# Optimization experiments

Hardware: AMD Instinct MI355X
Metric: run time of the kernel (lower is better)

Reference implementation:

```python
import jax, jax.numpy as jnp
import numpy as np

SEQ, B, I, H, L = 2048, 32, 1024, 1024, 2


def setup_inputs() -> dict:
    key = jax.random.key(0)
    ks = jax.random.split(key, 6)
    k = 1.0 / np.sqrt(H)
    x = jax.random.normal(ks[0], (SEQ, B, I), dtype=jnp.float32)
    h0 = jnp.zeros((L, B, H), dtype=jnp.float32)
    # layer 0 W_ih is [H, I]; with I == H all layers stack to [L, H, H]
    W_ih = jax.random.uniform(ks[1], (L, H, H), minval=-k, maxval=k, dtype=jnp.float32)
    W_hh = jax.random.uniform(ks[2], (L, H, H), minval=-k, maxval=k, dtype=jnp.float32)
    b_ih = jax.random.uniform(ks[3], (L, H), minval=-k, maxval=k, dtype=jnp.float32)
    b_hh = jax.random.uniform(ks[4], (L, H), minval=-k, maxval=k, dtype=jnp.float32)
    return {"x": x, "h0": h0, "W_ih": W_ih, "W_hh": W_hh, "b_ih": b_ih, "b_hh": b_hh}


def reference(x, h0, W_ih, W_hh, b_ih, b_hh):
    """Stacked tanh RNN, seq-first input [T, B, I]. Returns (h_history [T,B,H], h_T [L,B,H])."""
    num_layers = W_ih.shape[0]

    def step(h_prev, x_t):
        inp = x_t
        hs = []
        for l in range(num_layers):  # small fixed layer count
            a = (jnp.einsum('bd,cd->bc', inp, W_ih[l])
                 + jnp.einsum('bd,cd->bc', h_prev[l], W_hh[l])
                 + b_ih[l] + b_hh[l])
            hl = jnp.tanh(a)
            hs.append(hl)
            inp = hl
        h_new = jnp.stack(hs)  # [L, B, H]
        return h_new, h_new[-1]

    h_T, h_history = jax.lax.scan(step, h0, x)
    return h_history, h_T
```

## Files before the change

### kernel.cpp

```cpp
#include <hip/hip_runtime.h>
#include <stdint.h>

#define T_SEQ 2048
#define NB 32
#define NH 1024
#define HH (NH*NH)
#define HIST_ELEMS ((size_t)T_SEQ*NB*NH)
#define TEAM 32

typedef __attribute__((ext_vector_type(8))) short bf16x8;
typedef __attribute__((ext_vector_type(4))) float f32x4;
typedef __attribute__((ext_vector_type(4))) int   i32x4;
typedef __attribute__((ext_vector_type(2))) int   i32x2;
typedef __attribute__((ext_vector_type(4))) short s16x4;

__device__ __forceinline__ unsigned short bf16rne(float f){
  union { float f; unsigned u; } v; v.f = f;
  unsigned u = v.u;
  return (unsigned short)((u + 0x7FFFu + ((u >> 16) & 1u)) >> 16);
}
__device__ __forceinline__ float bf16tof(unsigned short s){
  union { unsigned u; float f; } v; v.u = ((unsigned)s) << 16; return v.f;
}
__device__ __forceinline__ float fast_tanh(float x){
  float ax = fabsf(x);
  float e  = __expf(-2.0f*ax);
  float t  = (1.0f - e) / (1.0f + e);
  return copysignf(t, x);
}

__device__ __forceinline__ i32x4 ld128_c(const void* p){
  i32x4 d;
  asm volatile("global_load_dwordx4 %0, %1, off sc0 sc1" : "=v"(d) : "v"(p) : "memory");
  return d;
}
__device__ __forceinline__ void st64_c(void* p, i32x2 v){
  asm volatile("global_store_dwordx2 %0, %1, off sc0 sc1" :: "v"(p), "v"(v) : "memory");
}
__device__ __forceinline__ void st32_c(void* p, unsigned v){
  asm volatile("global_store_dword %0, %1, off sc0 sc1" :: "v"(p), "v"(v) : "memory");
}
__device__ __forceinline__ unsigned ld32_c(const void* p){
  unsigned d;
  asm volatile("global_load_dword %0, %1, off sc0 sc1\n\ts_waitcnt vmcnt(0)"
               : "=v"(d) : "v"(p) : "memory");
  __builtin_amdgcn_sched_barrier(0);
  return d;
}
__device__ __forceinline__ void vmem_drain(){
  asm volatile("s_waitcnt vmcnt(0)" ::: "memory");
  __builtin_amdgcn_sched_barrier(0);
}

__global__ __launch_bounds__(256)
void pre_gemm(const float* __restrict__ x,
              const float* __restrict__ Wih,
              const float* __restrict__ bih,
              const float* __restrict__ bhh,
              _Float16* __restrict__ pre0)
{
  __shared__ float As[128][36];
  const int tid  = threadIdx.x;
  const int lane = tid & 63;
  const int wave = tid >> 6;
  const int l15  = lane & 15;
  const int l4   = lane >> 4;
  const int n0   = blockIdx.x * 128;
  const int m0   = blockIdx.y * 128;
  const int qm   = wave >> 1;
  const int qn   = wave & 1;

  f32x4 acc[4][4];
  #pragma unroll
  for (int i = 0; i < 4; ++i)
    #pragma unroll
    for (int j = 0; j < 4; ++j) acc[i][j] = (f32x4){0.f,0.f,0.f,0.f};

  const int sr = tid >> 1;
  const int sh = tid & 1;
  const float* xrow = x + (size_t)(m0 + sr)*NH + sh*16;

  for (int kb = 0; kb < 32; ++kb){
    __syncthreads();
    {
      const float* src = xrow + kb*32;
      f32x4 v0 = *(const f32x4*)(src + 0);
      f32x4 v1 = *(const f32x4*)(src + 4);
      f32x4 v2 = *(const f32x4*)(src + 8);
      f32x4 v3 = *(const f32x4*)(src + 12);
      float* dst = &As[sr][sh*16];
      *(f32x4*)(dst + 0)  = v0;
      *(f32x4*)(dst + 4)  = v1;
      *(f32x4*)(dst + 8)  = v2;
      *(f32x4*)(dst + 12) = v3;
    }
    __syncthreads();

    bf16x8 ahi[4], alo[4];
    #pragma unroll
    for (int mt = 0; mt < 4; ++mt){
      const float* ap = &As[64*qm + 16*mt + l15][l4*8];
      #pragma unroll
      for (int j = 0; j < 8; ++j){
        float a = ap[j];
        unsigned short hb = bf16rne(a);
        ahi[mt][j] = (short)hb;
        alo[mt][j] = (short)bf16rne(a - bf16tof(hb));
      }
    }
    #pragma unroll
    for (int nf = 0; nf < 4; ++nf){
      const int c = n0 + 64*qn + 16*nf + l15;
      const float* wp = Wih + (size_t)c*NH + kb*32 + l4*8;
      bf16x8 bf;
      #pragma unroll
      for (int j = 0; j < 8; ++j) bf[j] = (short)bf16rne(wp[j]);
      #pragma unroll
      for (int mt = 0; mt < 4; ++mt){
        acc[mt][nf] = __builtin_amdgcn_mfma_f32_16x16x32_bf16(ahi[mt], bf, acc[mt][nf], 0,0,0);
        acc[mt][nf] = __builtin_amdgcn_mfma_f32_16x16x32_bf16(alo[mt], bf, acc[mt][nf], 0,0,0);
      }
    }
  }

  #pragma unroll
  for (int nf = 0; nf < 4; ++nf){
    const int c = n0 + 64*qn + 16*nf + l15;
    const float bv = bih[c] + bhh[c];
    #pragma unroll
    for (int mt = 0; mt < 4; ++mt){
      const int mb = m0 + 64*qm + 16*mt + l4*4;
      #pragma unroll
      for (int j = 0; j < 4; ++j)
        pre0[(size_t)(mb + j)*NH + c] = (_Float16)(acc[mt][nf][j] + bv);
    }
  }
}

__global__ __launch_bounds__(256, 1)
void rnn_seq(const float* __restrict__ h0in,
             const float* __restrict__ Wih,
             const float* __restrict__ Whh,
             const float* __restrict__ bih,
             const float* __restrict__ bhh,
             const _Float16* __restrict__ pre0,
             float* __restrict__ dout,
             char* __restrict__ ws)
{
  const int tid  = threadIdx.x;
  const int lane = tid & 63;
  const int wave = tid >> 6;
  const int l15  = lane & 15;
  const int l4   = lane >> 4;

  unsigned* counts = (unsigned*)ws;
  unsigned* winner = (unsigned*)(ws + 64);
  unsigned* bcast  = (unsigned*)(ws + 128);
  unsigned* flags  = (unsigned*)(ws + 4096);
  char* h0buf = ws + 8192;
  char* h1buf = ws + 8192 + 131072;

  __shared__ unsigned sh_go, sh_rank, sh_base;

  if (tid == 0){
    unsigned xcc;
    asm volatile("s_getreg_b32 %0, hwreg(HW_REG_XCC_ID)" : "=s"(xcc));
    xcc &= 7u;
    unsigned slot = atomicAdd(&counts[xcc], 1u);
    unsigned go = 0, rank = 0, base = 0;
    if (slot < TEAM){
      if (slot == TEAM - 1) atomicCAS(winner, 0u, xcc + 1u);
      unsigned w = 0; long c = 0;
      for (;;){
        w = ld32_c(winner);
        if (w) break;
        if (++c > (1L << 20)) break;
        __builtin_amdgcn_s_sleep(8);
      }
      if (w == xcc + 1u){ go = 1; rank = slot; }
    }
    if (go){
      if (rank == 0){
        unsigned mx = 0;
        for (int i = 0; i < TEAM; ++i){ unsigned v = ld32_c(flags + i); if (v > mx) mx = v; }
        if (mx > 0xF0000000u) mx = 0;
        for (int i = 0; i < TEAM; ++i) st32_c(flags + i, mx);
        st32_c(bcast + 0, mx);
        vmem_drain();
        st32_c(bcast + 1, 1u);
        vmem_drain();
        base = mx;
      } else {
        long c = 0;
        for (;;){
          unsigned r = ld32_c(bcast + 1);
          if (r) break;
          if (++c > (1L << 23)) break;
          __builtin_amdgcn_s_sleep(2);
        }
        base = ld32_c(bcast + 0);
      }
    }
    sh_go = go; sh_rank = rank; sh_base = base;
  }
  __syncthreads();
  if (!sh_go) return;
  const unsigned rank = sh_rank;
  const unsigned base = sh_base;
  const int c0 = (int)rank * 32;

  bf16x8 wA[3][2][8];
  #pragma unroll
  for (int cf = 0; cf < 2; ++cf){
    const size_t row = (size_t)(c0 + cf*16 + l15) * NH;
    const float* s0 = Whh + row;
    const float* s1 = Wih + HH + row;
    const float* s2 = Whh + HH + row;
    #pragma unroll
    for (int s = 0; s < 8; ++s){
      const int k = wave*256 + s*32 + l4*8;
      #pragma unroll
      for (int j = 0; j < 8; ++j){
        wA[0][cf][s][j] = (short)bf16rne(s0[k+j]);
        wA[1][cf][s][j] = (short)bf16rne(s1[k+j]);
        wA[2][cf][s][j] = (short)bf16rne(s2[k+j]);
      }
    }
  }

  const int eb   = tid >> 3;
  const int ecb  = tid & 7;
  const int ecol = c0 + ecb*4;

  f32x4 bias1;
  #pragma unroll
  for (int j = 0; j < 4; ++j)
    bias1[j] = bih[NH + ecol + j] + bhh[NH + ecol + j];

  {
    const float* hs0 = h0in + (size_t)eb*NH + ecol;
    const float* hs1 = h0in + (size_t)NB*NH + (size_t)eb*NH + ecol;
    i32x2 p0, p1;
    p0[0] = (int)bf16rne(hs0[0]) | ((int)bf16rne(hs0[1]) << 16);
    p0[1] = (int)bf16rne(hs0[2]) | ((int)bf16rne(hs0[3]) << 16);
    p1[0] = (int)bf16rne(hs1[0]) | ((int)bf16rne(hs1[1]) << 16);
    p1[1] = (int)bf16rne(hs1[2]) | ((int)bf16rne(hs1[3]) << 16);
    st64_c(h0buf + 65536 + eb*2048 + ecol*2, p0);
    st64_c(h1buf + 65536 + eb*2048 + ecol*2, p1);
  }
  vmem_drain();
  __syncthreads();
  if (tid == 0) st32_c(flags + rank, base + 1u);

  __shared__ float scr[4][8][16][20];
  long spins = 0;

  for (int p = 0; p <= T_SEQ; ++p){
    const bool doL0 = (p < T_SEQ);
    const bool doL1 = (p >= 1);

    s16x4 praw = {0,0,0,0};
    if (doL0)
      praw = *(const s16x4*)(pre0 + (size_t)p*(NB*NH) + (size_t)eb*NH + ecol);

    if (wave == 0){
      const unsigned target = base + 1u + (unsigned)p;
      const unsigned* fp = flags + ((lane & 7) << 2);
      for (;;){
        i32x4 f = ld128_c(fp);
        vmem_drain();
        int ok = ((unsigned)f[0] >= target) && ((unsigned)f[1] >= target)
              && ((unsigned)f[2] >= target) && ((unsigned)f[3] >= target);
        if (__all(ok)) break;
        if (++spins > (1L << 25)) break;
        __builtin_amdgcn_s_sleep(1);
      }
    }
    __syncthreads();

    const char* h0rd = h0buf + ((p-1)&1)*65536;
    const char* h1rd = h1buf + ((p-2)&1)*65536;
    i32x4 g0[2][8], g1[2][8];
    #pragma unroll
    for (int bt = 0; bt < 2; ++bt){
      const int b = bt*16 + l15;
      #pragma unroll
      for (int s = 0; s < 8; ++s){
        const int d = wave*256 + s*32 + l4*8;
        g0[bt][s] = ld128_c(h0rd + b*2048 + d*2);
      }
    }
    if (doL1){
      #pragma unroll
      for (int bt = 0; bt < 2; ++bt){
        const int b = bt*16 + l15;
        #pragma unroll
        for (int s = 0; s < 8; ++s){
          const int d = wave*256 + s*32 + l4*8;
          g1[bt][s] = ld128_c(h1rd + b*2048 + d*2);
        }
      }
    }
    vmem_drain();

    f32x4 acc0[2][2] = {{{0,0,0,0},{0,0,0,0}},{{0,0,0,0},{0,0,0,0}}};
    f32x4 acc1[2][2] = {{{0,0,0,0},{0,0,0,0}},{{0,0,0,0},{0,0,0,0}}};
    #pragma unroll
    for (int cf = 0; cf < 2; ++cf){
      #pragma unroll
      for (int bt = 0; bt < 2; ++bt){
        #pragma unroll
        for (int s = 0; s < 8; ++s){
          bf16x8 b0 = __builtin_bit_cast(bf16x8, g0[bt][s]);
          if (doL0)
            acc0[cf][bt] = __builtin_amdgcn_mfma_f32_16x16x32_bf16(wA[0][cf][s], b0, acc0[cf][bt], 0,0,0);
          if (doL1){
            acc1[cf][bt] = __builtin_amdgcn_mfma_f32_16x16x32_bf16(wA[1][cf][s], b0, acc1[cf][bt], 0,0,0);
            bf16x8 b1 = __builtin_bit_cast(bf16x8, g1[bt][s]);
            acc1[cf][bt] = __builtin_amdgcn_mfma_f32_16x16x32_bf16(wA[2][cf][s], b1, acc1[cf][bt], 0,0,0);
          }
        }
      }
    }

    #pragma unroll
    for (int cf = 0; cf < 2; ++cf){
      #pragma unroll
      for (int bt = 0; bt < 2; ++bt){
        *(f32x4*)&scr[wave][(cf<<1)|bt][l15][l4*4]     = acc0[cf][bt];
        *(f32x4*)&scr[wave][4|(cf<<1)|bt][l15][l4*4]   = acc1[cf][bt];
      }
    }
    __syncthreads();

    const int fL0 = ((ecb >> 2) << 1) | (eb >> 4);
    f32x4 s0v = {0,0,0,0}, s1v = {0,0,0,0};
    #pragma unroll
    for (int w = 0; w < 4; ++w){
      s0v += *(const f32x4*)&scr[w][fL0][eb & 15][(ecb & 3)*4];
      s1v += *(const f32x4*)&scr[w][4|fL0][eb & 15][(ecb & 3)*4];
    }

    float hv0[4], hv1[4];
    if (doL0){
      union { s16x4 v; _Float16 h[4]; } pu; pu.v = praw;
      #pragma unroll
      for (int j = 0; j < 4; ++j)
        hv0[j] = fast_tanh(s0v[j] + (float)pu.h[j]);
      i32x2 pk;
      pk[0] = (int)bf16rne(hv0[0]) | ((int)bf16rne(hv0[1]) << 16);
      pk[1] = (int)bf16rne(hv0[2]) | ((int)bf16rne(hv0[3]) << 16);
      st64_c(h0buf + (p&1)*65536 + eb*2048 + ecol*2, pk);
    }
    if (doL1){
      #pragma unroll
      for (int j = 0; j < 4; ++j)
        hv1[j] = fast_tanh(s1v[j] + bias1[j]);
      i32x2 pk;
      pk[0] = (int)bf16rne(hv1[0]) | ((int)bf16rne(hv1[1]) << 16);
      pk[1] = (int)bf16rne(hv1[2]) | ((int)bf16rne(hv1[3]) << 16);
      st64_c(h1buf + ((p-1)&1)*65536 + eb*2048 + ecol*2, pk);
    }

    vmem_drain();
    __syncthreads();
    if (tid == 0) st32_c(flags + rank, base + 2u + (unsigned)p);

    if (doL1){
      f32x4 o = {hv1[0], hv1[1], hv1[2], hv1[3]};
      *(f32x4*)(dout + (size_t)(p-1)*(NB*NH) + (size_t)eb*NH + ecol) = o;
      if (p == T_SEQ)
        *(f32x4*)(dout + HIST_ELEMS + (size_t)NB*NH + (size_t)eb*NH + ecol) = o;
    }
    if (doL0 && p == T_SEQ-1){
      f32x4 o = {hv0[0], hv0[1], hv0[2], hv0[3]};
      *(f32x4*)(dout + HIST_ELEMS + (size_t)eb*NH + ecol) = o;
    }
  }
}

extern "C" void kernel_launch(void* const* d_in, const int* in_sizes, int n_in,
                              void* d_out, int out_size, void* d_ws, size_t ws_size,
                              hipStream_t stream)
{
  (void)in_sizes; (void)n_in; (void)out_size;
  const float* x   = (const float*)d_in[0];
  const float* h0  = (const float*)d_in[1];
  const float* Wih = (const float*)d_in[2];
  const float* Whh = (const float*)d_in[3];
  const float* bih = (const float*)d_in[4];
  const float* bhh = (const float*)d_in[5];
  float* out = (float*)d_out;
  char*  ws  = (char*)d_ws;

  const size_t PRE0_OFF = (size_t)1 << 20;
  const size_t NEED = PRE0_OFF + (size_t)T_SEQ*NB*NH*sizeof(_Float16);
  if (ws_size < NEED) return;

  _Float16* pre0 = (_Float16*)(ws + PRE0_OFF);

  hipMemsetAsync(ws, 0, 256, stream);
  pre_gemm<<<dim3(8, 512), 256, 0, stream>>>(x, Wih, bih, bhh, pre0);
  rnn_seq<<<dim3(512), 256, 0, stream>>>(h0, Wih, Whh, bih, bhh, pre0, out, ws);
}
```

Before: 15.42 ms.

## Replace flag barrier with tagged hidden-state words and launch only team blocks

The per-step flag barrier (stores, drain, flag write, then a wave spinning on every block's flag) is replaced by storing each bf16 hidden value next to a 16-bit step tag in 32-bit words. Readers poll the state buffer directly until all tags match the expected step. The XCC-team election is also dropped, so exactly 32 blocks are launched and rank comes from blockIdx. This removes a full round trip per step but doubles the state traffic, and it relies on all 32 blocks being co-resident and on the tags being written atomically with the data. A larger workspace region now has to be zeroed each call.

```diff
diff --git a/kernel.cpp b/kernel.cpp
--- a/kernel.cpp
+++ b/kernel.cpp
@@ -7,11 +7,11 @@
 #define HH (NH*NH)
 #define HIST_ELEMS ((size_t)T_SEQ*NB*NH)
 #define TEAM 32
+#define SLOT (NB*NH*4)
 
 typedef __attribute__((ext_vector_type(8))) short bf16x8;
 typedef __attribute__((ext_vector_type(4))) float f32x4;
 typedef __attribute__((ext_vector_type(4))) int   i32x4;
-typedef __attribute__((ext_vector_type(2))) int   i32x2;
 typedef __attribute__((ext_vector_type(4))) short s16x4;
 
 __device__ __forceinline__ unsigned short bf16rne(float f){
@@ -29,27 +29,17 @@
   return copysignf(t, x);
 }
 
-__device__ __forceinline__ i32x4 ld128_c(const void* p){
-  i32x4 d;
-  asm volatile("global_load_dwordx4 %0, %1, off sc0 sc1" : "=v"(d) : "v"(p) : "memory");
-  return d;
-}
-__device__ __forceinline__ void st64_c(void* p, i32x2 v){
-  asm volatile("global_store_dwordx2 %0, %1, off sc0 sc1" :: "v"(p), "v"(v) : "memory");
-}
-__device__ __forceinline__ void st32_c(void* p, unsigned v){
-  asm volatile("global_store_dword %0, %1, off sc0 sc1" :: "v"(p), "v"(v) : "memory");
-}
-__device__ __forceinline__ unsigned ld32_c(const void* p){
-  unsigned d;
-  asm volatile("global_load_dword %0, %1, off sc0 sc1\n\ts_waitcnt vmcnt(0)"
-               : "=v"(d) : "v"(p) : "memory");
-  __builtin_amdgcn_sched_barrier(0);
-  return d;
-}
-__device__ __forceinline__ void vmem_drain(){
-  asm volatile("s_waitcnt vmcnt(0)" ::: "memory");
-  __builtin_amdgcn_sched_barrier(0);
+__device__ __forceinline__ uint64_t ld_state(const uint64_t* p){
+  return __hip_atomic_load(p, __ATOMIC_RELAXED, __HIP_MEMORY_SCOPE_AGENT);
+}
+__device__ __forceinline__ void st_state(uint64_t* p, uint64_t v){
+  __hip_atomic_store(p, v, __ATOMIC_RELAXED, __HIP_MEMORY_SCOPE_AGENT);
+}
+
+__device__ __forceinline__ unsigned frag_word(uint64_t w, unsigned rep, unsigned &bad){
+  unsigned lo = (unsigned)w, hi = (unsigned)(w >> 32);
+  bad |= (((lo & 0xFFFFu) | (hi << 16)) ^ rep);
+  return (lo >> 16) | (hi & 0xFFFF0000u);
 }
 
 __global__ __launch_bounds__(256)
@@ -152,62 +142,11 @@
   const int wave = tid >> 6;
   const int l15  = lane & 15;
   const int l4   = lane >> 4;
-
-  unsigned* counts = (unsigned*)ws;
-  unsigned* winner = (unsigned*)(ws + 64);
-  unsigned* bcast  = (unsigned*)(ws + 128);
-  unsigned* flags  = (unsigned*)(ws + 4096);
-  char* h0buf = ws + 8192;
-  char* h1buf = ws + 8192 + 131072;
-
-  __shared__ unsigned sh_go, sh_rank, sh_base;
-
-  if (tid == 0){
-    unsigned xcc;
-    asm volatile("s_getreg_b32 %0, hwreg(HW_REG_XCC_ID)" : "=s"(xcc));
-    xcc &= 7u;
-    unsigned slot = atomicAdd(&counts[xcc], 1u);
-    unsigned go = 0, rank = 0, base = 0;
-    if (slot < TEAM){
-      if (slot == TEAM - 1) atomicCAS(winner, 0u, xcc + 1u);
-      unsigned w = 0; long c = 0;
-      for (;;){
-        w = ld32_c(winner);
-        if (w) break;
-        if (++c > (1L << 20)) break;
-        __builtin_amdgcn_s_sleep(8);
-      }
-      if (w == xcc + 1u){ go = 1; rank = slot; }
-    }
-    if (go){
-      if (rank == 0){
-        unsigned mx = 0;
-        for (int i = 0; i < TEAM; ++i){ unsigned v = ld32_c(flags + i); if (v > mx) mx = v; }
-        if (mx > 0xF0000000u) mx = 0;
-        for (int i = 0; i < TEAM; ++i) st32_c(flags + i, mx);
-        st32_c(bcast + 0, mx);
-        vmem_drain();
-        st32_c(bcast + 1, 1u);
-        vmem_drain();
-        base = mx;
-      } else {
-        long c = 0;
-        for (;;){
-          unsigned r = ld32_c(bcast + 1);
-          if (r) break;
-          if (++c > (1L << 23)) break;
-          __builtin_amdgcn_s_sleep(2);
-        }
-        base = ld32_c(bcast + 0);
-      }
-    }
-    sh_go = go; sh_rank = rank; sh_base = base;
-  }
-  __syncthreads();
-  if (!sh_go) return;
-  const unsigned rank = sh_rank;
-  const unsigned base = sh_base;
-  const int c0 = (int)rank * 32;
+  const int rank = blockIdx.x;
+  const int c0   = rank * 32;
+
+  char* H0 = ws + 4096;
+  char* H1 = ws + 4096 + 2*SLOT;
 
   bf16x8 wA[3][2][8];
   #pragma unroll
@@ -240,20 +179,21 @@
   {
     const float* hs0 = h0in + (size_t)eb*NH + ecol;
     const float* hs1 = h0in + (size_t)NB*NH + (size_t)eb*NH + ecol;
-    i32x2 p0, p1;
-    p0[0] = (int)bf16rne(hs0[0]) | ((int)bf16rne(hs0[1]) << 16);
-    p0[1] = (int)bf16rne(hs0[2]) | ((int)bf16rne(hs0[3]) << 16);
-    p1[0] = (int)bf16rne(hs1[0]) | ((int)bf16rne(hs1[1]) << 16);
-    p1[1] = (int)bf16rne(hs1[2]) | ((int)bf16rne(hs1[3]) << 16);
-    st64_c(h0buf + 65536 + eb*2048 + ecol*2, p0);
-    st64_c(h1buf + 65536 + eb*2048 + ecol*2, p1);
-  }
-  vmem_drain();
-  __syncthreads();
-  if (tid == 0) st32_c(flags + rank, base + 1u);
+    #pragma unroll
+    for (int half = 0; half < 2; ++half){
+      unsigned a0 = (((unsigned)bf16rne(hs0[2*half]))   << 16) | 1u;
+      unsigned a1 = (((unsigned)bf16rne(hs0[2*half+1])) << 16) | 1u;
+      unsigned b0 = (((unsigned)bf16rne(hs1[2*half]))   << 16) | 1u;
+      unsigned b1 = (((unsigned)bf16rne(hs1[2*half+1])) << 16) | 1u;
+      st_state((uint64_t*)(H0 + SLOT + (size_t)(eb*NH + ecol + 2*half)*4),
+               (uint64_t)a0 | ((uint64_t)a1 << 32));
+      st_state((uint64_t*)(H1 + SLOT + (size_t)(eb*NH + ecol + 2*half)*4),
+               (uint64_t)b0 | ((uint64_t)b1 << 32));
+    }
+  }
 
   __shared__ float scr[4][8][16][20];
-  long spins = 0;
+  long budget = 1L << 17;
 
   for (int p = 0; p <= T_SEQ; ++p){
     const bool doL0 = (p < T_SEQ);
@@ -263,45 +203,64 @@
     if (doL0)
       praw = *(const s16x4*)(pre0 + (size_t)p*(NB*NH) + (size_t)eb*NH + ecol);
 
-    if (wave == 0){
-      const unsigned target = base + 1u + (unsigned)p;
-      const unsigned* fp = flags + ((lane & 7) << 2);
-      for (;;){
-        i32x4 f = ld128_c(fp);
-        vmem_drain();
-        int ok = ((unsigned)f[0] >= target) && ((unsigned)f[1] >= target)
-              && ((unsigned)f[2] >= target) && ((unsigned)f[3] >= target);
-        if (__all(ok)) break;
-        if (++spins > (1L << 25)) break;
-        __builtin_amdgcn_s_sleep(1);
-      }
-    }
-    __syncthreads();
-
-    const char* h0rd = h0buf + ((p-1)&1)*65536;
-    const char* h1rd = h1buf + ((p-2)&1)*65536;
-    i32x4 g0[2][8], g1[2][8];
-    #pragma unroll
-    for (int bt = 0; bt < 2; ++bt){
-      const int b = bt*16 + l15;
-      #pragma unroll
-      for (int s = 0; s < 8; ++s){
-        const int d = wave*256 + s*32 + l4*8;
-        g0[bt][s] = ld128_c(h0rd + b*2048 + d*2);
-      }
-    }
-    if (doL1){
-      #pragma unroll
-      for (int bt = 0; bt < 2; ++bt){
-        const int b = bt*16 + l15;
+    const unsigned rep0 = (unsigned)(p + 1) * 0x10001u;
+    const unsigned rep1 = (unsigned)p       * 0x10001u;
+    const char* h0rd = H0 + (size_t)((p-1)&1)*SLOT;
+    const char* h1rd = H1 + (size_t)((p-2)&1)*SLOT;
+
+    i32x4 f0[2][8], f1[2][8];
+    bool need0 = true, need1 = doL1;
+    int round = 0;
+    while (need0 || need1){
+      if (need0){
+        unsigned bad = 0;
         #pragma unroll
-        for (int s = 0; s < 8; ++s){
-          const int d = wave*256 + s*32 + l4*8;
-          g1[bt][s] = ld128_c(h1rd + b*2048 + d*2);
+        for (int bt = 0; bt < 2; ++bt){
+          const uint64_t* rb =
+            (const uint64_t*)(h0rd + (size_t)(bt*16 + l15)*4096 + wave*1024 + l4*32);
+          #pragma unroll
+          for (int s = 0; s < 8; ++s){
+            uint64_t w0 = ld_state(rb + s*16 + 0);
+            uint64_t w1 = ld_state(rb + s*16 + 1);
+            uint64_t w2 = ld_state(rb + s*16 + 2);
+            uint64_t w3 = ld_state(rb + s*16 + 3);
+            i32x4 f;
+            f[0] = (int)frag_word(w0, rep0, bad);
+            f[1] = (int)frag_word(w1, rep0, bad);
+            f[2] = (int)frag_word(w2, rep0, bad);
+            f[3] = (int)frag_word(w3, rep0, bad);
+            f0[bt][s] = f;
+          }
         }
-      }
-    }
-    vmem_drain();
+        if (__all((int)(bad == 0))) need0 = false;
+      }
+      if (need1){
+        unsigned bad = 0;
+        #pragma unroll
+        for (int bt = 0; bt < 2; ++bt){
+          const uint64_t* rb =
+            (const uint64_t*)(h1rd + (size_t)(bt*16 + l15)*4096 + wave*1024 + l4*32);
+          #pragma unroll
+          for (int s = 0; s < 8; ++s){
+            uint64_t w0 = ld_state(rb + s*16 + 0);
+            uint64_t w1 = ld_state(rb + s*16 + 1);
+            uint64_t w2 = ld_state(rb + s*16 + 2);
+            uint64_t w3 = ld_state(rb + s*16 + 3);
+            i32x4 f;
+            f[0] = (int)frag_word(w0, rep1, bad);
+            f[1] = (int)frag_word(w1, rep1, bad);
+            f[2] = (int)frag_word(w2, rep1, bad);
+            f[3] = (int)frag_word(w3, rep1, bad);
+            f1[bt][s] = f;
+          }
+        }
+        if (__all((int)(bad == 0))) need1 = false;
+      }
+      if (need0 || need1){
+        if (--budget < 0) break;
+        if (++round > 2) __builtin_amdgcn_s_sleep(1);
+      }
+    }
 
     f32x4 acc0[2][2] = {{{0,0,0,0},{0,0,0,0}},{{0,0,0,0},{0,0,0,0}}};
     f32x4 acc1[2][2] = {{{0,0,0,0},{0,0,0,0}},{{0,0,0,0},{0,0,0,0}}};
@@ -311,24 +270,25 @@
       for (int bt = 0; bt < 2; ++bt){
         #pragma unroll
         for (int s = 0; s < 8; ++s){
-          bf16x8 b0 = __builtin_bit_cast(bf16x8, g0[bt][s]);
+          bf16x8 b0 = __builtin_bit_cast(bf16x8, f0[bt][s]);
           if (doL0)
             acc0[cf][bt] = __builtin_amdgcn_mfma_f32_16x16x32_bf16(wA[0][cf][s], b0, acc0[cf][bt], 0,0,0);
           if (doL1){
             acc1[cf][bt] = __builtin_amdgcn_mfma_f32_16x16x32_bf16(wA[1][cf][s], b0, acc1[cf][bt], 0,0,0);
-            bf16x8 b1 = __builtin_bit_cast(bf16x8, g1[bt][s]);
+            bf16x8 b1 = __builtin_bit_cast(bf16x8, f1[bt][s]);
             acc1[cf][bt] = __builtin_amdgcn_mfma_f32_16x16x32_bf16(wA[2][cf][s], b1, acc1[cf][bt], 0,0,0);
           }
         }
       }
     }
 
+    __syncthreads();
     #pragma unroll
     for (int cf = 0; cf < 2; ++cf){
       #pragma unroll
       for (int bt = 0; bt < 2; ++bt){
-        *(f32x4*)&scr[wave][(cf<<1)|bt][l15][l4*4]     = acc0[cf][bt];
-        *(f32x4*)&scr[wave][4|(cf<<1)|bt][l15][l4*4]   = acc1[cf][bt];
+        *(f32x4*)&scr[wave][(cf<<1)|bt][l15][l4*4]   = acc0[cf][bt];
+        *(f32x4*)&scr[wave][4|(cf<<1)|bt][l15][l4*4] = acc1[cf][bt];
       }
     }
     __syncthreads();
@@ -341,30 +301,34 @@
       s1v += *(const f32x4*)&scr[w][4|fL0][eb & 15][(ecb & 3)*4];
     }
 
+    const unsigned wtag0 = (unsigned)(p + 2);
+    const unsigned wtag1 = (unsigned)(p + 1);
     float hv0[4], hv1[4];
     if (doL0){
       union { s16x4 v; _Float16 h[4]; } pu; pu.v = praw;
       #pragma unroll
       for (int j = 0; j < 4; ++j)
         hv0[j] = fast_tanh(s0v[j] + (float)pu.h[j]);
-      i32x2 pk;
-      pk[0] = (int)bf16rne(hv0[0]) | ((int)bf16rne(hv0[1]) << 16);
-      pk[1] = (int)bf16rne(hv0[2]) | ((int)bf16rne(hv0[3]) << 16);
-      st64_c(h0buf + (p&1)*65536 + eb*2048 + ecol*2, pk);
+      char* wb = H0 + (size_t)(p&1)*SLOT + (size_t)(eb*NH + ecol)*4;
+      #pragma unroll
+      for (int half = 0; half < 2; ++half){
+        unsigned a0 = (((unsigned)bf16rne(hv0[2*half]))   << 16) | wtag0;
+        unsigned a1 = (((unsigned)bf16rne(hv0[2*half+1])) << 16) | wtag0;
+        st_state((uint64_t*)(wb + 8*half), (uint64_t)a0 | ((uint64_t)a1 << 32));
+      }
     }
     if (doL1){
       #pragma unroll
       for (int j = 0; j < 4; ++j)
         hv1[j] = fast_tanh(s1v[j] + bias1[j]);
-      i32x2 pk;
-      pk[0] = (int)bf16rne(hv1[0]) | ((int)bf16rne(hv1[1]) << 16);
-      pk[1] = (int)bf16rne(hv1[2]) | ((int)bf16rne(hv1[3]) << 16);
-      st64_c(h1buf + ((p-1)&1)*65536 + eb*2048 + ecol*2, pk);
-    }
-
-    vmem_drain();
-    __syncthreads();
-    if (tid == 0) st32_c(flags + rank, base + 2u + (unsigned)p);
+      char* wb = H1 + (size_t)((p-1)&1)*SLOT + (size_t)(eb*NH + ecol)*4;
+      #pragma unroll
+      for (int half = 0; half < 2; ++half){
+        unsigned a0 = (((unsigned)bf16rne(hv1[2*half]))   << 16) | wtag1;
+        unsigned a1 = (((unsigned)bf16rne(hv1[2*half+1])) << 16) | wtag1;
+        st_state((uint64_t*)(wb + 8*half), (uint64_t)a0 | ((uint64_t)a1 << 32));
+      }
+    }
 
     if (doL1){
       f32x4 o = {hv1[0], hv1[1], hv1[2], hv1[3]};
@@ -399,7 +363,7 @@
 
   _Float16* pre0 = (_Float16*)(ws + PRE0_OFF);
 
-  hipMemsetAsync(ws, 0, 256, stream);
+  hipMemsetAsync(ws, 0, 4096 + 4*(size_t)SLOT, stream);
   pre_gemm<<<dim3(8, 512), 256, 0, stream>>>(x, Wih, bih, bhh, pre0);
-  rnn_seq<<<dim3(512), 256, 0, stream>>>(h0, Wih, Whh, bih, bhh, pre0, out, ws);
-}
+  rnn_seq<<<dim3(TEAM), 256, 0, stream>>>(h0, Wih, Whh, bih, bhh, pre0, out, ws);
+}
```

Measured after the change: 46.18 ms. 3x slower.

## Replace XCC team election with direct 32-block launch and per-wave atomic flags

Applied to the files above, without the earlier changes.

The kernel now launches exactly 32 blocks instead of 512 and drops the XCC-local team election and base broadcast. Blocks therefore may land on different XCCs rather than sharing one. The per-step barrier now has each wave atomically bump its block's counter (each on its own 128-byte slot) and every wave poll all 32 counters itself. This removes two __syncthreads per step and the base-offset handshake. In exchange, cross-XCC traffic through coherent memory may be slower, and the spin now hot-polls before it sleeps.

```diff
diff --git a/kernel.cpp b/kernel.cpp
--- a/kernel.cpp
+++ b/kernel.cpp
@@ -36,9 +36,6 @@
 }
 __device__ __forceinline__ void st64_c(void* p, i32x2 v){
   asm volatile("global_store_dwordx2 %0, %1, off sc0 sc1" :: "v"(p), "v"(v) : "memory");
-}
-__device__ __forceinline__ void st32_c(void* p, unsigned v){
-  asm volatile("global_store_dword %0, %1, off sc0 sc1" :: "v"(p), "v"(v) : "memory");
 }
 __device__ __forceinline__ unsigned ld32_c(const void* p){
   unsigned d;
@@ -152,62 +149,12 @@
   const int wave = tid >> 6;
   const int l15  = lane & 15;
   const int l4   = lane >> 4;
-
-  unsigned* counts = (unsigned*)ws;
-  unsigned* winner = (unsigned*)(ws + 64);
-  unsigned* bcast  = (unsigned*)(ws + 128);
-  unsigned* flags  = (unsigned*)(ws + 4096);
-  char* h0buf = ws + 8192;
-  char* h1buf = ws + 8192 + 131072;
-
-  __shared__ unsigned sh_go, sh_rank, sh_base;
-
-  if (tid == 0){
-    unsigned xcc;
-    asm volatile("s_getreg_b32 %0, hwreg(HW_REG_XCC_ID)" : "=s"(xcc));
-    xcc &= 7u;
-    unsigned slot = atomicAdd(&counts[xcc], 1u);
-    unsigned go = 0, rank = 0, base = 0;
-    if (slot < TEAM){
-      if (slot == TEAM - 1) atomicCAS(winner, 0u, xcc + 1u);
-      unsigned w = 0; long c = 0;
-      for (;;){
-        w = ld32_c(winner);
-        if (w) break;
-        if (++c > (1L << 20)) break;
-        __builtin_amdgcn_s_sleep(8);
-      }
-      if (w == xcc + 1u){ go = 1; rank = slot; }
-    }
-    if (go){
-      if (rank == 0){
-        unsigned mx = 0;
-        for (int i = 0; i < TEAM; ++i){ unsigned v = ld32_c(flags + i); if (v > mx) mx = v; }
-        if (mx > 0xF0000000u) mx = 0;
-        for (int i = 0; i < TEAM; ++i) st32_c(flags + i, mx);
-        st32_c(bcast + 0, mx);
-        vmem_drain();
-        st32_c(bcast + 1, 1u);
-        vmem_drain();
-        base = mx;
-      } else {
-        long c = 0;
-        for (;;){
-          unsigned r = ld32_c(bcast + 1);
-          if (r) break;
-          if (++c > (1L << 23)) break;
-          __builtin_amdgcn_s_sleep(2);
-        }
-        base = ld32_c(bcast + 0);
-      }
-    }
-    sh_go = go; sh_rank = rank; sh_base = base;
-  }
-  __syncthreads();
-  if (!sh_go) return;
-  const unsigned rank = sh_rank;
-  const unsigned base = sh_base;
-  const int c0 = (int)rank * 32;
+  const int rank = blockIdx.x;
+  const int c0   = rank * 32;
+
+  unsigned* flags = (unsigned*)ws;
+  char* H0 = ws + 8192;
+  char* H1 = ws + 8192 + 131072;
 
   bf16x8 wA[3][2][8];
   #pragma unroll
@@ -245,12 +192,11 @@
     p0[1] = (int)bf16rne(hs0[2]) | ((int)bf16rne(hs0[3]) << 16);
     p1[0] = (int)bf16rne(hs1[0]) | ((int)bf16rne(hs1[1]) << 16);
     p1[1] = (int)bf16rne(hs1[2]) | ((int)bf16rne(hs1[3]) << 16);
-    st64_c(h0buf + 65536 + eb*2048 + ecol*2, p0);
-    st64_c(h1buf + 65536 + eb*2048 + ecol*2, p1);
+    st64_c(H0 + 65536 + eb*2048 + ecol*2, p0);
+    st64_c(H1 + 65536 + eb*2048 + ecol*2, p1);
   }
   vmem_drain();
-  __syncthreads();
-  if (tid == 0) st32_c(flags + rank, base + 1u);
+  if (lane == 0) atomicAdd(&flags[rank*32], 1u);
 
   __shared__ float scr[4][8][16][20];
   long spins = 0;
@@ -263,23 +209,20 @@
     if (doL0)
       praw = *(const s16x4*)(pre0 + (size_t)p*(NB*NH) + (size_t)eb*NH + ecol);
 
-    if (wave == 0){
-      const unsigned target = base + 1u + (unsigned)p;
-      const unsigned* fp = flags + ((lane & 7) << 2);
+    {
+      const unsigned target = 4u * (unsigned)(p + 1);
+      const unsigned* fp = flags + (lane & 31)*32;
       for (;;){
-        i32x4 f = ld128_c(fp);
-        vmem_drain();
-        int ok = ((unsigned)f[0] >= target) && ((unsigned)f[1] >= target)
-              && ((unsigned)f[2] >= target) && ((unsigned)f[3] >= target);
+        unsigned f = ld32_c(fp);
+        int ok = (lane >= 32) || (f >= target);
         if (__all(ok)) break;
-        if (++spins > (1L << 25)) break;
-        __builtin_amdgcn_s_sleep(1);
-      }
-    }
-    __syncthreads();
-
-    const char* h0rd = h0buf + ((p-1)&1)*65536;
-    const char* h1rd = h1buf + ((p-2)&1)*65536;
+        if (++spins > (1L << 21)) break;
+        if (spins > 4096) __builtin_amdgcn_s_sleep(1);
+      }
+    }
+
+    const char* h0rd = H0 + ((p-1)&1)*65536;
+    const char* h1rd = H1 + ((p-2)&1)*65536;
     i32x4 g0[2][8], g1[2][8];
     #pragma unroll
     for (int bt = 0; bt < 2; ++bt){
@@ -327,8 +270,8 @@
     for (int cf = 0; cf < 2; ++cf){
       #pragma unroll
       for (int bt = 0; bt < 2; ++bt){
-        *(f32x4*)&scr[wave][(cf<<1)|bt][l15][l4*4]     = acc0[cf][bt];
-        *(f32x4*)&scr[wave][4|(cf<<1)|bt][l15][l4*4]   = acc1[cf][bt];
+        *(f32x4*)&scr[wave][(cf<<1)|bt][l15][l4*4]   = acc0[cf][bt];
+        *(f32x4*)&scr[wave][4|(cf<<1)|bt][l15][l4*4] = acc1[cf][bt];
       }
     }
     __syncthreads();
@@ -350,7 +293,7 @@
       i32x2 pk;
       pk[0] = (int)bf16rne(hv0[0]) | ((int)bf16rne(hv0[1]) << 16);
       pk[1] = (int)bf16rne(hv0[2]) | ((int)bf16rne(hv0[3]) << 16);
-      st64_c(h0buf + (p&1)*65536 + eb*2048 + ecol*2, pk);
+      st64_c(H0 + (p&1)*65536 + eb*2048 + ecol*2, pk);
     }
     if (doL1){
       #pragma unroll
@@ -359,12 +302,11 @@
       i32x2 pk;
       pk[0] = (int)bf16rne(hv1[0]) | ((int)bf16rne(hv1[1]) << 16);
       pk[1] = (int)bf16rne(hv1[2]) | ((int)bf16rne(hv1[3]) << 16);
-      st64_c(h1buf + ((p-1)&1)*65536 + eb*2048 + ecol*2, pk);
+      st64_c(H1 + ((p-1)&1)*65536 + eb*2048 + ecol*2, pk);
     }
 
     vmem_drain();
-    __syncthreads();
-    if (tid == 0) st32_c(flags + rank, base + 2u + (unsigned)p);
+    if (lane == 0) atomicAdd(&flags[rank*32], 1u);
 
     if (doL1){
       f32x4 o = {hv1[0], hv1[1], hv1[2], hv1[3]};
@@ -399,7 +341,7 @@
 
   _Float16* pre0 = (_Float16*)(ws + PRE0_OFF);
 
-  hipMemsetAsync(ws, 0, 256, stream);
+  hipMemsetAsync(ws, 0, 4096, stream);
   pre_gemm<<<dim3(8, 512), 256, 0, stream>>>(x, Wih, bih, bhh, pre0);
-  rnn_seq<<<dim3(512), 256, 0, stream>>>(h0, Wih, Whh, bih, bhh, pre0, out, ws);
-}
+  rnn_seq<<<dim3(TEAM), 256, 0, stream>>>(h0, Wih, Whh, bih, bhh, pre0, out, ws);
+}
```

After: 15.75 ms. 1.02x slower.
